# Kernel optimization log

Hardware: AMD Instinct MI355X
Metric: run time of the kernel (lower is better)

Reference implementation:

```python
import jax, jax.numpy as jnp
import numpy as np

B, T, C, H = 2, 2048, 1024, 16
HD = C // H  # head dim = 64


def setup_inputs() -> dict:
    key = jax.random.key(0)
    k1, k2, k3 = jax.random.split(key, 3)
    scale_in = 1.0 / np.sqrt(C)
    x = jax.random.normal(k1, (B, T, C), dtype=jnp.float32)
    w_qkv = jax.random.normal(k2, (C, 3 * C), dtype=jnp.float32) * scale_in
    b_qkv = jnp.zeros((3 * C,), dtype=jnp.float32)
    w_out = jax.random.normal(k3, (C, C), dtype=jnp.float32) * scale_in
    b_out = jnp.zeros((C,), dtype=jnp.float32)
    return {"x": x, "w_qkv": w_qkv, "b_qkv": b_qkv, "w_out": w_out, "b_out": b_out}


def reference(x, w_qkv, b_qkv, w_out, b_out):
    Bq, Tq, Cq = x.shape
    qkv = x @ w_qkv + b_qkv                       # [B,T,3C]
    q, k, v = jnp.split(qkv, 3, axis=-1)          # each [B,T,C]
    # [B,T,C] -> [B,H,T,HD]
    q = q.reshape(Bq, Tq, H, HD).transpose(0, 2, 1, 3)
    k = k.reshape(Bq, Tq, H, HD).transpose(0, 2, 1, 3)
    v = v.reshape(Bq, Tq, H, HD).transpose(0, 2, 1, 3)
    scale = 1.0 / np.sqrt(HD)
    scores = jnp.einsum("bhqd,bhkd->bhqk", q, k) * scale  # [B,H,T,T]
    causal = jnp.tril(jnp.ones((Tq, Tq), dtype=bool))
    scores = jnp.where(causal[None, None], scores, jnp.finfo(scores.dtype).min)
    attn = jax.nn.softmax(scores, axis=-1)
    y = jnp.einsum("bhqk,bhkd->bhqd", attn, v)    # [B,H,T,HD]
    y = y.transpose(0, 2, 1, 3).reshape(Bq, Tq, Cq)
    return y @ w_out + b_out
```

## Files before the change

kernel.cpp:

```cpp
#include <hip/hip_runtime.h>
#include <hip/hip_bf16.h>


#define B_ 2
#define T_ 2048
#define C_ 1024
#define H_ 16
#define HD_ 64
#define M_ (B_ * T_)
#define N3_ (3 * C_)
#define QK2_ 2048
#define QSCALE 0.18033688f

typedef __attribute__((ext_vector_type(8))) short short8;
typedef __attribute__((ext_vector_type(4))) short short4v;
typedef __attribute__((ext_vector_type(4))) float floatx4;

__device__ __forceinline__ unsigned short f2b(float f) {
    __hip_bfloat16 h = __float2bfloat16(f);
    return *reinterpret_cast<unsigned short*>(&h);
}

__device__ __forceinline__ void glds16(const void* g, void* l) {
    __builtin_amdgcn_global_load_lds(
        (const __attribute__((address_space(1))) void*)g,
        (__attribute__((address_space(3))) void*)l, 16, 0, 0);
}

__global__ __launch_bounds__(256) void pack_bf16(
    const float* __restrict__ src, unsigned short* __restrict__ dst) {
    int i = (blockIdx.x * 256 + threadIdx.x) * 4;
    float4 v = *reinterpret_cast<const float4*>(src + i);
    short4v s;
    s[0] = (short)f2b(v.x); s[1] = (short)f2b(v.y);
    s[2] = (short)f2b(v.z); s[3] = (short)f2b(v.w);
    *reinterpret_cast<short4v*>(dst + i) = s;
}

__global__ __launch_bounds__(256) void transpose_pack(
    const float* __restrict__ src, unsigned short* __restrict__ dst,
    int K, int N) {
    __shared__ float t[32][33];
    const int n0 = blockIdx.x * 32, k0 = blockIdx.y * 32;
    const int tx = threadIdx.x & 31, ty = threadIdx.x >> 5;
#pragma unroll
    for (int i = 0; i < 4; i++)
        t[ty + i * 8][tx] = src[(size_t)(k0 + ty + i * 8) * N + n0 + tx];
    __syncthreads();
#pragma unroll
    for (int i = 0; i < 4; i++)
        dst[(size_t)(n0 + ty + i * 8) * K + k0 + tx] = f2b(t[tx][ty + i * 8]);
}

template<int EPI, int BN>
__global__ __launch_bounds__(256) void gemm_glds(
    const unsigned short* __restrict__ A, const unsigned short* __restrict__ Bt,
    const float* __restrict__ bias, void* __restrict__ Cp,
    unsigned short* __restrict__ vtp, int M, int N, int K) {
    constexpr int NI = BN / 32;
    __shared__ __align__(16) unsigned short Al[128 * 64];
    __shared__ __align__(16) unsigned short Bl[BN * 64];

    const int tid  = threadIdx.x;
    const int lane = tid & 63;
    const int w    = tid >> 6;
    const int c16  = lane & 15;
    const int quad = lane >> 4;
    const int n0 = blockIdx.x * BN;
    const int m0 = blockIdx.y * 128;
    const int wm = (w >> 1) * 64;
    const int wn = (w & 1) * (BN / 2);

    floatx4 acc[4][NI] = {};

    const int srow = lane >> 3;
    const int sch  = ((lane & 7) ^ srow) * 8;
    const unsigned short* ag = A + (size_t)(m0 + w * 32 + srow) * K + sch;
    const unsigned short* bg = Bt + (size_t)(n0 + w * (BN / 4) + srow) * K + sch;

    const int s7 = c16 & 7;

    for (int k0 = 0; k0 < K; k0 += 64) {
        __syncthreads();
#pragma unroll
        for (int i = 0; i < 4; i++)
            glds16(ag + k0 + (size_t)(i * 8) * K, &Al[(w * 32 + i * 8) * 64]);
#pragma unroll
        for (int i = 0; i < BN / 32; i++)
            glds16(bg + k0 + (size_t)(i * 8) * K,
                   &Bl[(w * (BN / 4) + i * 8) * 64]);
        __syncthreads();

        short8 af[4][2], bf[NI][2];
#pragma unroll
        for (int im = 0; im < 4; im++)
#pragma unroll
            for (int kk = 0; kk < 2; kk++)
                af[im][kk] = *reinterpret_cast<const short8*>(
                    &Al[(wm + im * 16 + c16) * 64 + ((kk * 4 + quad) ^ s7) * 8]);
#pragma unroll
        for (int in = 0; in < NI; in++)
#pragma unroll
            for (int kk = 0; kk < 2; kk++)
                bf[in][kk] = *reinterpret_cast<const short8*>(
                    &Bl[(wn + in * 16 + c16) * 64 + ((kk * 4 + quad) ^ s7) * 8]);
#pragma unroll
        for (int im = 0; im < 4; im++)
#pragma unroll
            for (int in = 0; in < NI; in++)
#pragma unroll
                for (int kk = 0; kk < 2; kk++)
                    acc[im][in] = __builtin_amdgcn_mfma_f32_16x16x32_bf16(
                        af[im][kk], bf[in][kk], acc[im][in], 0, 0, 0);
    }

    const int ncol = n0 + wn;
    float bv[NI];
#pragma unroll
    for (int in = 0; in < NI; in++) bv[in] = bias[ncol + in * 16 + c16];

    if (EPI == 0) {
        float* C = (float*)Cp;
#pragma unroll
        for (int im = 0; im < 4; im++)
#pragma unroll
            for (int r = 0; r < 4; r++) {
                int row = m0 + wm + im * 16 + quad * 4 + r;
#pragma unroll
                for (int in = 0; in < NI; in++)
                    C[(size_t)row * N + ncol + in * 16 + c16] =
                        acc[im][in][r] + bv[in];
            }
    } else {
        if (ncol < 2 * C_) {
            const float fac = (ncol < C_) ? QSCALE : 1.0f;
            unsigned short* qkp = (unsigned short*)Cp;
#pragma unroll
            for (int im = 0; im < 4; im++)
#pragma unroll
                for (int r = 0; r < 4; r++) {
                    int row = m0 + wm + im * 16 + quad * 4 + r;
#pragma unroll
                    for (int in = 0; in < NI; in++)
                        qkp[(size_t)row * QK2_ + ncol + in * 16 + c16] =
                            f2b((acc[im][in][r] + bv[in]) * fac);
                }
        } else {
#pragma unroll
            for (int im = 0; im < 4; im++) {
                int row0 = m0 + wm + im * 16 + quad * 4;
                int b  = row0 >> 11;
                int t0 = row0 & (T_ - 1);
#pragma unroll
                for (int in = 0; in < NI; in++) {
                    int dfull = ncol - 2 * C_ + in * 16 + c16;
                    short4v sv;
#pragma unroll
                    for (int r = 0; r < 4; r++)
                        sv[r] = (short)f2b(acc[im][in][r] + bv[in]);
                    *reinterpret_cast<short4v*>(
                        &vtp[(((size_t)(b << 10) + dfull) << 11) + t0]) = sv;
                }
            }
        }
    }
}

template<bool MASKED>
__device__ __forceinline__ void attn_tile(
    short8 af0, short8 af1,
    const unsigned short* __restrict__ Kl,
    const unsigned short* __restrict__ Vl,
    unsigned short* __restrict__ pw,
    floatx4 O[4], float& l,
    int row0, int kb, int c16, int quad) {
    const floatx4 z = {0.f, 0.f, 0.f, 0.f};
    const int sx  = c16 & 7;
    const int ch0 = (quad ^ sx) * 8;
    const int ch1 = ((quad + 4) ^ sx) * 8;
    floatx4 s[4];
#pragma unroll
    for (int nt = 0; nt < 4; nt++) {
        const int rb = (nt * 16 + c16) * 64;
        short8 k0 = *reinterpret_cast<const short8*>(&Kl[rb + ch0]);
        short8 k1 = *reinterpret_cast<const short8*>(&Kl[rb + ch1]);
        floatx4 t = __builtin_amdgcn_mfma_f32_16x16x32_bf16(k0, af0, z, 0, 0, 0);
        s[nt] = __builtin_amdgcn_mfma_f32_16x16x32_bf16(k1, af1, t, 0, 0, 0);
    }
    const int qrow = row0 + c16;
#pragma unroll
    for (int nt = 0; nt < 4; nt++) {
        short4v p4;
#pragma unroll
        for (int r = 0; r < 4; r++) {
            float p;
            if (MASKED) {
                int key = kb + nt * 16 + quad * 4 + r;
                p = (key <= qrow) ? exp2f(s[nt][r]) : 0.f;
            } else {
                p = exp2f(s[nt][r]);
            }
            l += p;
            p4[r] = (short)f2b(p);
        }
        *reinterpret_cast<short4v*>(&pw[c16 * 72 + nt * 16 + quad * 4]) = p4;
    }
    short8 pf0 = *reinterpret_cast<const short8*>(&pw[c16 * 72 + quad * 8]);
    short8 pf1 = *reinterpret_cast<const short8*>(&pw[c16 * 72 + 32 + quad * 8]);
#pragma unroll
    for (int nt = 0; nt < 4; nt++) {
        const int rb = (nt * 16 + c16) * 64;
        short8 v0 = *reinterpret_cast<const short8*>(&Vl[rb + ch0]);
        short8 v1 = *reinterpret_cast<const short8*>(&Vl[rb + ch1]);
        floatx4 t = __builtin_amdgcn_mfma_f32_16x16x32_bf16(pf0, v0, O[nt], 0, 0, 0);
        O[nt] = __builtin_amdgcn_mfma_f32_16x16x32_bf16(pf1, v1, t, 0, 0, 0);
    }
}

__global__ __launch_bounds__(256) void attn_mfma(
    const unsigned short* __restrict__ qk,
    const unsigned short* __restrict__ vt,
    unsigned short* __restrict__ y) {
    __shared__ __align__(16) unsigned short Kl[64 * 64];
    __shared__ __align__(16) unsigned short Vl[64 * 64];
    __shared__ __align__(16) unsigned short Pl[4 * 16 * 72];

    const int tid  = threadIdx.x;
    const int lane = tid & 63;
    const int w    = tid >> 6;
    const int c16  = lane & 15;
    const int quad = lane >> 4;
    const int bh = blockIdx.x & 31;
    const int t  = 31 - (blockIdx.x >> 5);
    const int b  = bh >> 4;
    const int h  = bh & 15;
    const int row0 = (4 * t + w) * 16;
    const int nch  = t + 1;

    const unsigned short* qrow = qk + (size_t)b * T_ * QK2_ + h * HD_;
    const unsigned short* krow = qrow + C_;
    const unsigned short* vrow = vt + ((size_t)bh << 6) * T_;

    short8 af0 = *reinterpret_cast<const short8*>(
        qrow + (size_t)(row0 + c16) * QK2_ + quad * 8);
    short8 af1 = *reinterpret_cast<const short8*>(
        qrow + (size_t)(row0 + c16) * QK2_ + 32 + quad * 8);

    floatx4 O[4] = {};
    float l = 0.f;
    unsigned short* pw = &Pl[w * 16 * 72];

    const int r8 = lane >> 3;
    const int sw = ((lane & 7) ^ r8) * 8;

    for (int c = 0; c < nch; c++) {
        const int kb = c * 64;
        __syncthreads();
#pragma unroll
        for (int i = 0; i < 2; i++) {
            const int row = w * 16 + i * 8 + r8;
            glds16(krow + (size_t)(kb + row) * QK2_ + sw,
                   &Kl[(w * 16 + i * 8) * 64]);
            glds16(vrow + (size_t)row * T_ + kb + sw,
                   &Vl[(w * 16 + i * 8) * 64]);
        }
        __syncthreads();

        if (c + 1 < nch)
            attn_tile<false>(af0, af1, Kl, Vl, pw, O, l, row0, kb, c16, quad);
        else
            attn_tile<true>(af0, af1, Kl, Vl, pw, O, l, row0, kb, c16, quad);
    }

    l += __shfl_xor(l, 16);
    l += __shfl_xor(l, 32);
    float lr[4];
#pragma unroll
    for (int r = 0; r < 4; r++)
        lr[r] = __shfl(l, quad * 4 + r);

#pragma unroll
    for (int nt = 0; nt < 4; nt++)
#pragma unroll
        for (int r = 0; r < 4; r++) {
            float val = O[nt][r] / fmaxf(lr[r], 1e-30f);
            y[((size_t)b * T_ + row0 + quad * 4 + r) * C_ + h * HD_ + nt * 16 + c16] =
                f2b(val);
        }
}

extern "C" void kernel_launch(void* const* d_in, const int* in_sizes, int n_in,
                              void* d_out, int out_size, void* d_ws, size_t ws_size,
                              hipStream_t stream) {
    const float* x     = (const float*)d_in[0];
    const float* w_qkv = (const float*)d_in[1];
    const float* b_qkv = (const float*)d_in[2];
    const float* w_out = (const float*)d_in[3];
    const float* b_out = (const float*)d_in[4];
    float* out = (float*)d_out;

    unsigned short* qkb = (unsigned short*)d_ws;
    unsigned short* vtb = qkb + (size_t)M_ * QK2_;
    unsigned short* yb  = vtb + (size_t)B_ * H_ * HD_ * T_;
    unsigned short* wt1 = yb + (size_t)M_ * C_;
    unsigned short* wt2 = wt1 + (size_t)N3_ * C_;
    unsigned short* xb  = wt2 + (size_t)C_ * C_;

    pack_bf16<<<M_ * C_ / 1024, 256, 0, stream>>>(x, xb);
    transpose_pack<<<dim3(N3_ / 32, C_ / 32), 256, 0, stream>>>(w_qkv, wt1, C_, N3_);
    transpose_pack<<<dim3(C_ / 32, C_ / 32), 256, 0, stream>>>(w_out, wt2, C_, C_);

    dim3 g1(N3_ / 128, M_ / 128);
    gemm_glds<1, 128><<<g1, 256, 0, stream>>>(xb, wt1, b_qkv, qkb, vtb, M_, N3_, C_);

    attn_mfma<<<B_ * H_ * 32, 256, 0, stream>>>(qkb, vtb, yb);

    dim3 g2(C_ / 64, M_ / 128);
    gemm_glds<0, 64><<<g2, 256, 0, stream>>>(yb, wt2, b_out, out, nullptr, M_, C_, C_);
}
```

Before: 180.0 us.

## Halve attention block size, merge prep kernels, pad P tile stride

The attention kernel now uses 128-thread blocks with two waves, each block covering 32 query rows, and launches twice as many blocks so causal work is split more finely and more blocks fit per CU. In each block one wave loads the K tile and the other loads the V tile. The three preprocessing kernels (x cast, two weight transposes) are merged into one launch to save launch overhead. The P scratch row stride changes from 72 to 76 to alter the LDS bank mapping. The trade-off is that each K/V tile is now reused by only two waves, which raises the global load traffic per unit of work.

```diff
diff --git a/kernel.cpp b/kernel.cpp
--- a/kernel.cpp
+++ b/kernel.cpp
@@ -11,6 +11,7 @@
 #define N3_ (3 * C_)
 #define QK2_ 2048
 #define QSCALE 0.18033688f
+#define PSTR 76
 
 typedef __attribute__((ext_vector_type(8))) short short8;
 typedef __attribute__((ext_vector_type(4))) short short4v;
@@ -27,29 +28,40 @@
         (__attribute__((address_space(3))) void*)l, 16, 0, 0);
 }
 
-__global__ __launch_bounds__(256) void pack_bf16(
-    const float* __restrict__ src, unsigned short* __restrict__ dst) {
-    int i = (blockIdx.x * 256 + threadIdx.x) * 4;
-    float4 v = *reinterpret_cast<const float4*>(src + i);
-    short4v s;
-    s[0] = (short)f2b(v.x); s[1] = (short)f2b(v.y);
-    s[2] = (short)f2b(v.z); s[3] = (short)f2b(v.w);
-    *reinterpret_cast<short4v*>(dst + i) = s;
-}
-
-__global__ __launch_bounds__(256) void transpose_pack(
-    const float* __restrict__ src, unsigned short* __restrict__ dst,
-    int K, int N) {
+__global__ __launch_bounds__(256) void prep(
+    const float* __restrict__ x, const float* __restrict__ w_qkv,
+    const float* __restrict__ w_out, unsigned short* __restrict__ xb,
+    unsigned short* __restrict__ wt1, unsigned short* __restrict__ wt2) {
     __shared__ float t[32][33];
-    const int n0 = blockIdx.x * 32, k0 = blockIdx.y * 32;
-    const int tx = threadIdx.x & 31, ty = threadIdx.x >> 5;
+    const int bi = blockIdx.x;
+    const int tid = threadIdx.x;
+    if (bi < 4096) {
+        int i = (bi * 256 + tid) * 4;
+        float4 v = *reinterpret_cast<const float4*>(x + i);
+        short4v s;
+        s[0] = (short)f2b(v.x); s[1] = (short)f2b(v.y);
+        s[2] = (short)f2b(v.z); s[3] = (short)f2b(v.w);
+        *reinterpret_cast<short4v*>(xb + i) = s;
+        return;
+    }
+    const float* src; unsigned short* dst; int n0, k0, N;
+    if (bi < 4096 + 3072) {
+        int u = bi - 4096;
+        src = w_qkv; dst = wt1; N = N3_;
+        n0 = (u % 96) * 32; k0 = (u / 96) * 32;
+    } else {
+        int u = bi - 7168;
+        src = w_out; dst = wt2; N = C_;
+        n0 = (u & 31) * 32; k0 = (u >> 5) * 32;
+    }
+    const int tx = tid & 31, ty = tid >> 5;
 #pragma unroll
     for (int i = 0; i < 4; i++)
         t[ty + i * 8][tx] = src[(size_t)(k0 + ty + i * 8) * N + n0 + tx];
     __syncthreads();
 #pragma unroll
     for (int i = 0; i < 4; i++)
-        dst[(size_t)(n0 + ty + i * 8) * K + k0 + tx] = f2b(t[tx][ty + i * 8]);
+        dst[(size_t)(n0 + ty + i * 8) * C_ + k0 + tx] = f2b(t[tx][ty + i * 8]);
 }
 
 template<int EPI, int BN>
@@ -203,10 +215,10 @@
             l += p;
             p4[r] = (short)f2b(p);
         }
-        *reinterpret_cast<short4v*>(&pw[c16 * 72 + nt * 16 + quad * 4]) = p4;
-    }
-    short8 pf0 = *reinterpret_cast<const short8*>(&pw[c16 * 72 + quad * 8]);
-    short8 pf1 = *reinterpret_cast<const short8*>(&pw[c16 * 72 + 32 + quad * 8]);
+        *reinterpret_cast<short4v*>(&pw[c16 * PSTR + nt * 16 + quad * 4]) = p4;
+    }
+    short8 pf0 = *reinterpret_cast<const short8*>(&pw[c16 * PSTR + quad * 8]);
+    short8 pf1 = *reinterpret_cast<const short8*>(&pw[c16 * PSTR + 32 + quad * 8]);
 #pragma unroll
     for (int nt = 0; nt < 4; nt++) {
         const int rb = (nt * 16 + c16) * 64;
@@ -217,13 +229,13 @@
     }
 }
 
-__global__ __launch_bounds__(256) void attn_mfma(
+__global__ __launch_bounds__(128) void attn_mfma(
     const unsigned short* __restrict__ qk,
     const unsigned short* __restrict__ vt,
     unsigned short* __restrict__ y) {
     __shared__ __align__(16) unsigned short Kl[64 * 64];
     __shared__ __align__(16) unsigned short Vl[64 * 64];
-    __shared__ __align__(16) unsigned short Pl[4 * 16 * 72];
+    __shared__ __align__(16) unsigned short Pl[2 * 16 * PSTR];
 
     const int tid  = threadIdx.x;
     const int lane = tid & 63;
@@ -231,11 +243,11 @@
     const int c16  = lane & 15;
     const int quad = lane >> 4;
     const int bh = blockIdx.x & 31;
-    const int t  = 31 - (blockIdx.x >> 5);
+    const int j  = 63 - (blockIdx.x >> 5);
     const int b  = bh >> 4;
     const int h  = bh & 15;
-    const int row0 = (4 * t + w) * 16;
-    const int nch  = t + 1;
+    const int row0 = (2 * j + w) * 16;
+    const int nch  = j / 2 + 1;
 
     const unsigned short* qrow = qk + (size_t)b * T_ * QK2_ + h * HD_;
     const unsigned short* krow = qrow + C_;
@@ -248,7 +260,7 @@
 
     floatx4 O[4] = {};
     float l = 0.f;
-    unsigned short* pw = &Pl[w * 16 * 72];
+    unsigned short* pw = &Pl[w * 16 * PSTR];
 
     const int r8 = lane >> 3;
     const int sw = ((lane & 7) ^ r8) * 8;
@@ -256,13 +268,16 @@
     for (int c = 0; c < nch; c++) {
         const int kb = c * 64;
         __syncthreads();
-#pragma unroll
-        for (int i = 0; i < 2; i++) {
-            const int row = w * 16 + i * 8 + r8;
-            glds16(krow + (size_t)(kb + row) * QK2_ + sw,
-                   &Kl[(w * 16 + i * 8) * 64]);
-            glds16(vrow + (size_t)row * T_ + kb + sw,
-                   &Vl[(w * 16 + i * 8) * 64]);
+        if (w == 0) {
+#pragma unroll
+            for (int i = 0; i < 8; i++)
+                glds16(krow + (size_t)(kb + i * 8 + r8) * QK2_ + sw,
+                       &Kl[(i * 8) * 64]);
+        } else {
+#pragma unroll
+            for (int i = 0; i < 8; i++)
+                glds16(vrow + (size_t)(i * 8 + r8) * T_ + kb + sw,
+                       &Vl[(i * 8) * 64]);
         }
         __syncthreads();
 
@@ -306,14 +321,12 @@
     unsigned short* wt2 = wt1 + (size_t)N3_ * C_;
     unsigned short* xb  = wt2 + (size_t)C_ * C_;
 
-    pack_bf16<<<M_ * C_ / 1024, 256, 0, stream>>>(x, xb);
-    transpose_pack<<<dim3(N3_ / 32, C_ / 32), 256, 0, stream>>>(w_qkv, wt1, C_, N3_);
-    transpose_pack<<<dim3(C_ / 32, C_ / 32), 256, 0, stream>>>(w_out, wt2, C_, C_);
+    prep<<<4096 + 3072 + 1024, 256, 0, stream>>>(x, w_qkv, w_out, xb, wt1, wt2);
 
     dim3 g1(N3_ / 128, M_ / 128);
     gemm_glds<1, 128><<<g1, 256, 0, stream>>>(xb, wt1, b_qkv, qkb, vtb, M_, N3_, C_);
 
-    attn_mfma<<<B_ * H_ * 32, 256, 0, stream>>>(qkb, vtb, yb);
+    attn_mfma<<<B_ * H_ * 64, 128, 0, stream>>>(qkb, vtb, yb);
 
     dim3 g2(C_ / 64, M_ / 128);
     gemm_glds<0, 64><<<g2, 256, 0, stream>>>(yb, wt2, b_out, out, nullptr, M_, C_, C_);
```

Measured after the change: 189.7 us. 5.4% more time.
